# Optimization experiments

Hardware: AMD Instinct MI355X
Metric: run time of the kernel (lower is better)

Reference implementation:

```python
import jax, jax.numpy as jnp
import numpy as np

N, F, H, C, E, DEPTH = 4096, 1433, 32, 7, 131072, 3
RATIO = 0.5

def dense_adj(edge_index, n):
    # undirected, unweighted, no self loops (Planetoid-style graph)
    A = jnp.zeros((n, n), jnp.float32).at[edge_index[0], edge_index[1]].set(1.0)
    A = jnp.maximum(A, A.T)
    return A * (1.0 - jnp.eye(n, dtype=jnp.float32))

def gcn(x, A, W, b):
    # GCNConv(improved=True): A_hat = A + 2I, symmetric degree normalization
    n = A.shape[0]
    Ah = A + 2.0 * jnp.eye(n, dtype=A.dtype)
    deg = Ah.sum(axis=1)
    dinv = jnp.where(deg > 0, jax.lax.rsqrt(deg), 0.0)
    return (dinv[:, None] * Ah * dinv[None, :]) @ (x @ W) + b

def augment(A):
    # PyG GraphUNet.augment_adj: add self loops, A @ A, remove self loops
    n = A.shape[0]
    Ai = A + jnp.eye(n, dtype=A.dtype)
    return (Ai @ Ai) * (1.0 - jnp.eye(n, dtype=A.dtype))

def topk_pool(x, A, p):
    # TopKPooling(ratio=0.5) with tanh score nonlinearity
    score = jnp.tanh((x @ p) / jnp.linalg.norm(p))
    k = int(np.ceil(RATIO * x.shape[0]))  # static under jit
    vals, perm = jax.lax.top_k(score, k)
    return x[perm] * vals[:, None], A[perm][:, perm], perm

def net_forward(x, A, Wi, bi, down_W, down_b, pool_p, up_W, up_b, Wf, bf):
    # eval mode: dropout_adj(p=0.2) and F.dropout(p=0.92) are identity
    x = jax.nn.relu(gcn(x, A, Wi, bi))
    # GraphUNet down path
    h = jax.nn.relu(gcn(x, A, down_W[0], down_b[0]))
    xs, As, perms = [h], [A], []
    cur_A = A
    for i in range(1, DEPTH + 1):
        Aaug = augment(cur_A)
        h, cur_A, perm = topk_pool(h, Aaug, pool_p[i - 1])
        h = jax.nn.relu(gcn(h, cur_A, down_W[i], down_b[i]))
        if i < DEPTH:
            xs.append(h)
            As.append(cur_A)
        perms.append(perm)
    # up path with sum residuals
    for i in range(DEPTH):
        j = DEPTH - 1 - i
        up = jnp.zeros_like(xs[j]).at[perms[j]].set(h)
        h = xs[j] + up
        h = gcn(h, As[j], up_W[i], up_b[i])
        if i < DEPTH - 1:
            h = jax.nn.relu(h)
    x = jax.nn.relu(h)
    out = gcn(x, A, Wf, bf)
    return jax.nn.log_softmax(out, axis=1)

def setup_inputs():
    key = jax.random.key(0)
    ks = jax.random.split(key, 8)
    return {
        "x": jax.random.normal(ks[0], (N, F), dtype=jnp.float32),
        "edge_index": jax.random.randint(ks[1], (2, E), 0, N),
        "Wi": jax.random.normal(ks[2], (F, H), dtype=jnp.float32) / np.float32(np.sqrt(F)),
        "bi": jnp.zeros((H,), jnp.float32),
        "down_W": jax.random.normal(ks[3], (DEPTH + 1, H, H), dtype=jnp.float32) / np.float32(np.sqrt(H)),
        "down_b": jnp.zeros((DEPTH + 1, H), jnp.float32),
        "pool_p": jax.random.normal(ks[4], (DEPTH, H), dtype=jnp.float32),
        "up_W": jax.random.normal(ks[5], (DEPTH, H, H), dtype=jnp.float32) / np.float32(np.sqrt(H)),
        "up_b": jnp.zeros((DEPTH, H), jnp.float32),
        "Wf": jax.random.normal(ks[6], (H, C), dtype=jnp.float32) / np.float32(np.sqrt(H)),
        "bf": jnp.zeros((C,), jnp.float32),
    }

def reference(x, edge_index, Wi, bi, down_W, down_b, pool_p, up_W, up_b, Wf, bf):
    A = dense_adj(edge_index, N)
    return net_forward(x, A, Wi, bi, down_W, down_b, pool_p, up_W, up_b, Wf, bf)
```

## Files before the change

### kernel.cpp

```cpp
#include <hip/hip_runtime.h>
#include <hip/hip_bf16.h>
#include <cstdint>

#define N_NODES 4096
#define F_IN    1433
#define N_EDGE  131072

typedef short short8v __attribute__((ext_vector_type(8)));
typedef float f32x4 __attribute__((ext_vector_type(4)));

#define GLOBAL_AS __attribute__((address_space(1)))
#define LDS_AS    __attribute__((address_space(3)))

__device__ __forceinline__ void gload_lds16(const void* g, void* l) {
  __builtin_amdgcn_global_load_lds((const GLOBAL_AS void*)g, (LDS_AS void*)l, 16, 0, 0);
}

__device__ __forceinline__ float bf16_to_f32(unsigned short u) {
  union { unsigned u; float f; } c;
  c.u = ((unsigned)u) << 16;
  return c.f;
}

__device__ __forceinline__ unsigned short f32_to_bf16_rne(float f) {
  union { float f; unsigned u; } c; c.f = f;
  unsigned u = c.u;
  return (unsigned short)((u + 0x7FFFu + ((u >> 16) & 1u)) >> 16);
}


__global__ void scatter_edges_k(const int* __restrict__ e0, const int* __restrict__ e1,
                                unsigned short* __restrict__ Ab, int n, int ne) {
  int t = blockIdx.x * 256 + threadIdx.x;
  if (t >= ne) return;
  int u = e0[t], v = e1[t];
  if (u != v) {
    Ab[(size_t)u * n + v] = 0x3F80;
    Ab[(size_t)v * n + u] = 0x3F80;
  }
}

__global__ void deg_dinv_bf16_k(const unsigned short* __restrict__ A,
                                float* __restrict__ dinv, int n) {
  int wid  = (blockIdx.x * blockDim.x + threadIdx.x) >> 6;
  int lane = threadIdx.x & 63;
  if (wid >= n) return;
  const unsigned short* row = A + (size_t)wid * n;
  float s = 0.f;
  for (int j = lane * 8; j < n; j += 512) {
    uint4 v = *(const uint4*)(row + j);
    s += bf16_to_f32((unsigned short)(v.x & 0xffff)) + bf16_to_f32((unsigned short)(v.x >> 16));
    s += bf16_to_f32((unsigned short)(v.y & 0xffff)) + bf16_to_f32((unsigned short)(v.y >> 16));
    s += bf16_to_f32((unsigned short)(v.z & 0xffff)) + bf16_to_f32((unsigned short)(v.z >> 16));
    s += bf16_to_f32((unsigned short)(v.w & 0xffff)) + bf16_to_f32((unsigned short)(v.w >> 16));
  }
#pragma unroll
  for (int off = 32; off > 0; off >>= 1) s += __shfl_down(s, off, 64);
  if (lane == 0) {
    float d = s + 2.0f;
    dinv[wid] = d > 0.f ? 1.0f / sqrtf(d) : 0.f;
  }
}

__global__ void deg_dinv_f32_k(const float* __restrict__ A, float* __restrict__ dinv, int n) {
  int wid  = (blockIdx.x * blockDim.x + threadIdx.x) >> 6;
  int lane = threadIdx.x & 63;
  if (wid >= n) return;
  const float* row = A + (size_t)wid * n;
  float s = 0.f;
  for (int j = lane * 4; j < n; j += 256) {
    float4 v = *(const float4*)(row + j);
    s += (v.x + v.y) + (v.z + v.w);
  }
#pragma unroll
  for (int off = 32; off > 0; off >>= 1) s += __shfl_down(s, off, 64);
  if (lane == 0) {
    float d = s + 2.0f;
    dinv[wid] = d > 0.f ? 1.0f / sqrtf(d) : 0.f;
  }
}


__global__ void gather_rows_bf16_k(const unsigned short* __restrict__ src,
                                   const int* __restrict__ perm,
                                   unsigned short* __restrict__ dst, int K, int cbits) {
  size_t t = (size_t)blockIdx.x * 256 + threadIdx.x;
  int r  = (int)(t >> cbits);
  int c8 = (int)(t & ((1u << cbits) - 1));
  uint4 v = *(const uint4*)(src + (size_t)perm[r] * K + c8 * 8);
  *(uint4*)(dst + t * 8) = v;
}

__global__ void gather_rows_f32_k(const float* __restrict__ src,
                                  const int* __restrict__ perm,
                                  float* __restrict__ dst, int K, int cbits) {
  size_t t = (size_t)blockIdx.x * 256 + threadIdx.x;
  int r  = (int)(t >> cbits);
  int c4 = (int)(t & ((1u << cbits) - 1));
  float4 v = *(const float4*)(src + (size_t)perm[r] * K + c4 * 4);
  *(float4*)(dst + t * 4) = v;
}


__device__ __forceinline__ void block_map(int bid, int nb, int& bx, int& by) {
  if (nb == 16) {
    int xcd = bid & 7, idx = bid >> 3;
    by = (xcd >> 1) * 4 + (idx >> 3);
    bx = (xcd & 1) * 8 + (idx & 7);
  } else if (nb == 8) {
    int xcd = bid & 7, idx = bid >> 3;
    by = (xcd >> 1) * 2 + (idx >> 2);
    bx = (xcd & 1) * 4 + (idx & 3);
  } else {
    bx = bid % nb; by = bid / nb;
  }
}

__global__ __launch_bounds__(512) void gemm_bf16_pool_k(
    const __hip_bfloat16* __restrict__ Ap, const int* __restrict__ perm,
    float* __restrict__ outF, unsigned short* __restrict__ outB, int M, int K) {
  __shared__ short lds[2][2][128 * 32];
  int nb = M >> 7;
  int bx, by; block_map(blockIdx.x, nb, bx, by);
  int row0 = by << 7, col0 = bx << 7;
  int tid = threadIdx.x;
  int wv = tid >> 6, ln = tid & 63;
  int lr = ln & 15, kh = ln >> 4;
  int wr = wv >> 2, wc = wv & 3;

  f32x4 acc[4][2] = {};

  auto stage = [&](int buf, int k0) {
#pragma unroll
    for (int t = 0; t < 2; ++t) {
      int rbase = t ? col0 : row0;
      int row = tid >> 2, colb = (tid & 3) * 16;
      const char* g = (const char*)(Ap + (size_t)(rbase + row) * K + k0) + colb;
      gload_lds16(g, (char*)&lds[buf][t][0] + wv * 1024);
    }
  };

  int nt = K >> 5;
  stage(0, 0);
  int cur = 0;
  for (int kt = 0; kt < nt; ++kt) {
    __syncthreads();
    if (kt + 1 < nt) stage(cur ^ 1, (kt + 1) << 5);
    const short* AbL = &lds[cur][0][0];
    const short* BbL = &lds[cur][1][0];
    short8v af[4], bfr[2];
#pragma unroll
    for (int m = 0; m < 4; ++m)
      af[m] = *(const short8v*)(AbL + (wr * 64 + m * 16 + lr) * 32 + kh * 8);
#pragma unroll
    for (int q = 0; q < 2; ++q)
      bfr[q] = *(const short8v*)(BbL + (wc * 32 + q * 16 + lr) * 32 + kh * 8);
#pragma unroll
    for (int m = 0; m < 4; ++m)
#pragma unroll
      for (int q = 0; q < 2; ++q)
        acc[m][q] = __builtin_amdgcn_mfma_f32_16x16x32_bf16(af[m], bfr[q], acc[m][q], 0, 0, 0);
    cur ^= 1;
  }

#pragma unroll
  for (int q = 0; q < 2; ++q) {
    int col = col0 + wc * 32 + q * 16 + lr;
    int pc  = perm[col];
#pragma unroll
    for (int m = 0; m < 4; ++m) {
      int rb = row0 + wr * 64 + m * 16 + kh * 4;
#pragma unroll
      for (int r = 0; r < 4; ++r) {
        int row = rb + r;
        float v = acc[m][q][r] +
                  2.0f * bf16_to_f32(((const unsigned short*)Ap)[(size_t)row * K + pc]);
        if (row == col) v = 0.f;
        if (outF) outF[(size_t)row * M + col] = v;
        if (outB) {
          union { float f; unsigned u; } c2; c2.f = v;
          outB[(size_t)row * M + col] = (unsigned short)(c2.u >> 16);
        }
      }
    }
  }
}


__global__ __launch_bounds__(256) void gemm_f32_pool_k(
    const float* __restrict__ Ap, const int* __restrict__ perm,
    float* __restrict__ outF, int M, int K) {
  __shared__ float As[32][33];
  __shared__ float Bs[32][33];
  int nb = M >> 5;
  int bx = blockIdx.x % nb, by = blockIdx.x / nb;
  int row0 = by << 5, col0 = bx << 5;
  int tid = threadIdx.x;
  int tr = tid >> 4, tc = tid & 15;
  int lr = tid >> 3, lq = (tid & 7) * 4;
  float acc[2][2] = {};
  for (int k0 = 0; k0 < K; k0 += 32) {
    float4 av = *(const float4*)(Ap + (size_t)(row0 + lr) * K + k0 + lq);
    float4 bv = *(const float4*)(Ap + (size_t)(col0 + lr) * K + k0 + lq);
    __syncthreads();
    As[lq + 0][lr] = av.x; As[lq + 1][lr] = av.y;
    As[lq + 2][lr] = av.z; As[lq + 3][lr] = av.w;
    Bs[lq + 0][lr] = bv.x; Bs[lq + 1][lr] = bv.y;
    Bs[lq + 2][lr] = bv.z; Bs[lq + 3][lr] = bv.w;
    __syncthreads();
#pragma unroll
    for (int k = 0; k < 32; ++k) {
      float2 a = *(const float2*)&As[k][tr * 2];
      float2 b = *(const float2*)&Bs[k][tc * 2];
      acc[0][0] += a.x * b.x; acc[0][1] += a.x * b.y;
      acc[1][0] += a.y * b.x; acc[1][1] += a.y * b.y;
    }
  }
#pragma unroll
  for (int j = 0; j < 2; ++j) {
    int col = col0 + tc * 2 + j;
    int pc = perm[col];
#pragma unroll
    for (int i = 0; i < 2; ++i) {
      int row = row0 + tr * 2 + i;
      float v = acc[i][j] + 2.0f * Ap[(size_t)row * K + pc];
      if (row == col) v = 0.f;
      outF[(size_t)row * M + col] = v;
    }
  }
}

template <int K2>
__global__ void xw_scale_k(const float* __restrict__ X, const float* __restrict__ W,
                           const float* __restrict__ dinv, float* __restrict__ Z,
                           int n, int K1, int relu_in) {
  __shared__ float Xs[8][128];
  int tx = threadIdx.x, ty = threadIdx.y;
  int i0 = blockIdx.x * 8;
  int tid = ty * 32 + tx;
  float acc = 0.f;
  for (int k0 = 0; k0 < K1; k0 += 128) {
    __syncthreads();
#pragma unroll
    for (int l = 0; l < 4; ++l) {
      int idx = tid + l * 256;
      int r = idx >> 7, kk = idx & 127;
      float xv = (k0 + kk < K1) ? X[(size_t)(i0 + r) * K1 + k0 + kk] : 0.f;
      if (relu_in) xv = fmaxf(xv, 0.f);
      Xs[r][kk] = xv;
    }
    __syncthreads();
    if (tx < K2) {
      int lim = min(128, K1 - k0);
      for (int kk = 0; kk < lim; ++kk)
        acc += Xs[ty][kk] * W[(size_t)(k0 + kk) * K2 + tx];
    }
  }
  if (tx < K2) Z[(size_t)(i0 + ty) * K2 + tx] = dinv[i0 + ty] * acc;
}


template <int RELU, int PRESCALED>
__global__ __launch_bounds__(256) void xsplit_k(const float* __restrict__ X,
                                                const float* __restrict__ dinv,
                                                unsigned short* __restrict__ T0,
                                                unsigned short* __restrict__ T1,
                                                unsigned short* __restrict__ T2, int n) {
  __shared__ float Xs[64][33];
  int tid = threadIdx.x;
  int i0 = blockIdx.x * 64;
#pragma unroll
  for (int l = 0; l < 2; ++l) {
    int idx = tid + l * 256;
    int r = idx >> 3, c4 = (idx & 7) * 4;
    float4 v = *(const float4*)(X + (size_t)(i0 + r) * 32 + c4);
    if (RELU) {
      v.x = fmaxf(v.x, 0.f); v.y = fmaxf(v.y, 0.f);
      v.z = fmaxf(v.z, 0.f); v.w = fmaxf(v.w, 0.f);
    }
    float s = PRESCALED ? 1.f : dinv[i0 + r];
    Xs[r][c4 + 0] = s * v.x; Xs[r][c4 + 1] = s * v.y;
    Xs[r][c4 + 2] = s * v.z; Xs[r][c4 + 3] = s * v.w;
  }
  __syncthreads();
  int c = tid >> 3, ib = (tid & 7) * 8;
  unsigned h0[4], h1[4], h2[4];
#pragma unroll
  for (int u = 0; u < 8; u += 2) {
    unsigned short a0, a1, b0, b1, c0, c1;
    {
      float v = Xs[ib + u][c];
      a0 = f32_to_bf16_rne(v); float r0 = v - bf16_to_f32(a0);
      b0 = f32_to_bf16_rne(r0); float r1 = r0 - bf16_to_f32(b0);
      c0 = f32_to_bf16_rne(r1);
    }
    {
      float v = Xs[ib + u + 1][c];
      a1 = f32_to_bf16_rne(v); float r0 = v - bf16_to_f32(a1);
      b1 = f32_to_bf16_rne(r0); float r1 = r0 - bf16_to_f32(b1);
      c1 = f32_to_bf16_rne(r1);
    }
    h0[u >> 1] = (unsigned)a0 | ((unsigned)a1 << 16);
    h1[u >> 1] = (unsigned)b0 | ((unsigned)b1 << 16);
    h2[u >> 1] = (unsigned)c0 | ((unsigned)c1 << 16);
  }
  size_t o = (size_t)c * n + i0 + ib;
  *(uint4*)(T0 + o) = make_uint4(h0[0], h0[1], h0[2], h0[3]);
  *(uint4*)(T1 + o) = make_uint4(h1[0], h1[1], h1[2], h1[3]);
  *(uint4*)(T2 + o) = make_uint4(h2[0], h2[1], h2[2], h2[3]);
}


template <int HAS_W, int HCO, int LOGSM>
__global__ __launch_bounds__(512) void agg_mfma_k(
    const unsigned short* __restrict__ Aadj,
    const unsigned short* __restrict__ T0, const unsigned short* __restrict__ T1,
    const unsigned short* __restrict__ T2,
    const float* __restrict__ X, const float* __restrict__ dinv,
    const float* __restrict__ W, const float* __restrict__ bias,
    float* __restrict__ out, int n, int prescaled, int relu_in, int relu_out) {
  __shared__ float yw[8][32][17];
  __shared__ float Ws[32][32];
  __shared__ float ytot[32][17];
  __shared__ float Os[16][8];
  __shared__ float bs[32];
  int tid = threadIdx.x;
  int wv = tid >> 6, ln = tid & 63;
  int lr = ln & 15, kh = ln >> 4;
  int node0 = blockIdx.x * 16;

  if (HAS_W) {
    if (HCO == 32) {
#pragma unroll
      for (int l = 0; l < 2; ++l) {
        int idx = tid + l * 512;
        Ws[idx >> 5][idx & 31] = W[idx];
      }
    } else {
      if (tid < 32 * HCO) Ws[tid / HCO][tid % HCO] = W[tid];
    }
  }
  if (tid < HCO) bs[tid] = bias[tid];

  int kper = n >> 3;
  int kbeg = wv * kper;
  const unsigned short* Ar = Aadj + (size_t)(node0 + lr) * n + kh * 8;
  const unsigned short* t0 = T0 + (size_t)lr * n + kh * 8;
  const unsigned short* t1 = T1 + (size_t)lr * n + kh * 8;
  const unsigned short* t2 = T2 + (size_t)lr * n + kh * 8;
  const size_t m16 = (size_t)16 * n;

  f32x4 acc0 = {0.f, 0.f, 0.f, 0.f}, acc1 = {0.f, 0.f, 0.f, 0.f};
  for (int k = kbeg; k < kbeg + kper; k += 32) {
    short8v b   = *(const short8v*)(Ar + k);
    short8v a00 = *(const short8v*)(t0 + k);
    short8v a01 = *(const short8v*)(t0 + m16 + k);
    short8v a10 = *(const short8v*)(t1 + k);
    short8v a11 = *(const short8v*)(t1 + m16 + k);
    short8v a20 = *(const short8v*)(t2 + k);
    short8v a21 = *(const short8v*)(t2 + m16 + k);
    acc0 = __builtin_amdgcn_mfma_f32_16x16x32_bf16(a00, b, acc0, 0, 0, 0);
    acc1 = __builtin_amdgcn_mfma_f32_16x16x32_bf16(a01, b, acc1, 0, 0, 0);
    acc0 = __builtin_amdgcn_mfma_f32_16x16x32_bf16(a10, b, acc0, 0, 0, 0);
    acc1 = __builtin_amdgcn_mfma_f32_16x16x32_bf16(a11, b, acc1, 0, 0, 0);
    acc0 = __builtin_amdgcn_mfma_f32_16x16x32_bf16(a20, b, acc0, 0, 0, 0);
    acc1 = __builtin_amdgcn_mfma_f32_16x16x32_bf16(a21, b, acc1, 0, 0, 0);
  }
#pragma unroll
  for (int r = 0; r < 4; ++r) {
    yw[wv][kh * 4 + r][lr]      = acc0[r];
    yw[wv][16 + kh * 4 + r][lr] = acc1[r];
  }
  __syncthreads();

  {
    int c = tid >> 4, i = tid & 15;
    float ysum = 0.f;
#pragma unroll
    for (int w = 0; w < 8; ++w) ysum += yw[w][c][i];
    int node = node0 + i;
    float di = dinv[node];
    float xi = X[(size_t)node * 32 + c];
    if (relu_in) xi = fmaxf(xi, 0.f);
    float si = prescaled ? 1.f : di;
    float yt = di * (ysum + 2.f * si * xi);
    if (!HAS_W) {
      yt += bs[c];
      if (relu_out) yt = fmaxf(yt, 0.f);
      out[(size_t)node * 32 + c] = yt;
    } else {
      ytot[c][i] = yt;
    }
  }
  if (!HAS_W) return;
  __syncthreads();

  if (HCO == 32) {
    int i = tid >> 5, cf = tid & 31;
    float o = bs[cf];
#pragma unroll
    for (int c = 0; c < 32; ++c) o += ytot[c][i] * Ws[c][cf];
    if (relu_out) o = fmaxf(o, 0.f);
    out[(size_t)(node0 + i) * 32 + cf] = o;
  } else {
    int i = tid >> 5, cf = tid & 31;
    if (cf < HCO) {
      float o = bs[cf];
#pragma unroll
      for (int c = 0; c < 32; ++c) o += ytot[c][i] * Ws[c][cf];
      Os[i][cf] = o;
    }
    __syncthreads();
    if (LOGSM) {
      if (tid < 16) {
        int node = node0 + tid;
        float m = Os[tid][0];
#pragma unroll
        for (int c2 = 1; c2 < 7; ++c2) m = fmaxf(m, Os[tid][c2]);
        float ss = 0.f;
#pragma unroll
        for (int c2 = 0; c2 < 7; ++c2) ss += expf(Os[tid][c2] - m);
        float ls = logf(ss);
#pragma unroll
        for (int c2 = 0; c2 < 7; ++c2) out[(size_t)node * 7 + c2] = Os[tid][c2] - m - ls;
      }
    } else {
      if (cf < HCO) out[(size_t)(node0 + i) * 7 + cf] = Os[i][cf];
    }
  }
}


template <int BF16A, int HCO, int HAS_W, int LOGSM>
__global__ __launch_bounds__(256) void gcn_fused_k(
    const void* __restrict__ Av, const float* __restrict__ X,
    const float* __restrict__ dinv, const float* __restrict__ W,
    const float* __restrict__ bias, float* __restrict__ out,
    int n, int prescaled, int relu_in, int relu_out) {
  __shared__ float As[16][68];
  __shared__ float Xs[64][32];
  __shared__ float Ws[32][32];
  __shared__ float Ys[16][33];
  __shared__ float Os[16][8];
  __shared__ float bs[32];
  int tid = threadIdx.x;
  int rt = tid >> 4, cg = tid & 15;
  int row0 = blockIdx.x * 16;

  if (HAS_W) {
    if (HCO == 32) {
#pragma unroll
      for (int l = 0; l < 4; ++l) {
        int idx = tid + l * 256;
        Ws[idx >> 5][idx & 31] = W[idx];
      }
    } else {
      if (tid < 32 * HCO) Ws[tid / HCO][tid % HCO] = W[tid];
    }
  }
  if (tid < HCO) bs[tid] = bias[tid];

  float acc0 = 0.f, acc1 = 0.f;
  for (int j0 = 0; j0 < n; j0 += 64) {
    __syncthreads();
    {
      int r = tid >> 4, q = (tid & 15) * 4;
      if (BF16A) {
        ushort4 a4 = *(const ushort4*)((const unsigned short*)Av + (size_t)(row0 + r) * n + j0 + q);
        As[r][q + 0] = bf16_to_f32(a4.x);
        As[r][q + 1] = bf16_to_f32(a4.y);
        As[r][q + 2] = bf16_to_f32(a4.z);
        As[r][q + 3] = bf16_to_f32(a4.w);
      } else {
        *(float4*)&As[r][q] = *(const float4*)((const float*)Av + (size_t)(row0 + r) * n + j0 + q);
      }
    }
#pragma unroll
    for (int l = 0; l < 2; ++l) {
      int f = tid + l * 256;
      int r = f >> 3, q = (f & 7) * 4;
      float4 v = *(const float4*)(X + (size_t)(j0 + r) * 32 + q);
      if (relu_in) {
        v.x = fmaxf(v.x, 0.f); v.y = fmaxf(v.y, 0.f);
        v.z = fmaxf(v.z, 0.f); v.w = fmaxf(v.w, 0.f);
      }
      float s = prescaled ? 1.f : dinv[j0 + r];
      Xs[r][q + 0] = s * v.x; Xs[r][q + 1] = s * v.y;
      Xs[r][q + 2] = s * v.z; Xs[r][q + 3] = s * v.w;
    }
    __syncthreads();
#pragma unroll
    for (int j = 0; j < 64; ++j) {
      float av = As[rt][j];
      float2 zv = *(const float2*)&Xs[j][cg * 2];
      acc0 += av * zv.x;
      acc1 += av * zv.y;
    }
  }

  int row = row0 + rt;
  float di = dinv[row];
  int c0 = cg * 2;
  float xa = X[(size_t)row * 32 + c0], xb = X[(size_t)row * 32 + c0 + 1];
  if (relu_in) { xa = fmaxf(xa, 0.f); xb = fmaxf(xb, 0.f); }
  float s_i = prescaled ? 1.f : di;
  float y0 = di * (acc0 + 2.f * s_i * xa);
  float y1 = di * (acc1 + 2.f * s_i * xb);

  if (!HAS_W) {
    y0 += bs[c0]; y1 += bs[c0 + 1];
    if (relu_out) { y0 = fmaxf(y0, 0.f); y1 = fmaxf(y1, 0.f); }
    *(float2*)(out + (size_t)row * 32 + c0) = make_float2(y0, y1);
    return;
  }

  Ys[rt][c0] = y0; Ys[rt][c0 + 1] = y1;
  __syncthreads();
  if (HCO == 32) {
    float o0 = bs[c0], o1 = bs[c0 + 1];
#pragma unroll
    for (int c = 0; c < 32; ++c) {
      float yv = Ys[rt][c];
      o0 += yv * Ws[c][c0];
      o1 += yv * Ws[c][c0 + 1];
    }
    if (relu_out) { o0 = fmaxf(o0, 0.f); o1 = fmaxf(o1, 0.f); }
    *(float2*)(out + (size_t)row * 32 + c0) = make_float2(o0, o1);
  } else {
    if (cg < HCO) {
      float o = bs[cg];
#pragma unroll
      for (int c = 0; c < 32; ++c) o += Ys[rt][c] * Ws[c][cg];
      Os[rt][cg] = o;
    }
    __syncthreads();
    if (LOGSM) {
      if (cg == 0) {
        float m = Os[rt][0];
#pragma unroll
        for (int c = 1; c < 7; ++c) m = fmaxf(m, Os[rt][c]);
        float ss = 0.f;
#pragma unroll
        for (int c = 0; c < 7; ++c) ss += expf(Os[rt][c] - m);
        float ls = logf(ss);
#pragma unroll
        for (int c = 0; c < 7; ++c) out[(size_t)row * 7 + c] = Os[rt][c] - m - ls;
      }
    } else {
      if (cg < HCO) out[(size_t)row * 7 + cg] = Os[rt][cg];
    }
  }
}


__global__ void score_k(const float* __restrict__ h, const float* __restrict__ p,
                        float* __restrict__ score, int n) {
  int i = blockIdx.x * 256 + threadIdx.x;
  if (i >= n) return;
  float s = 0.f, pn = 0.f;
#pragma unroll
  for (int c = 0; c < 32; ++c) {
    float pc = p[c];
    s += h[(size_t)i * 32 + c] * pc;
    pn += pc * pc;
  }
  score[i] = tanhf(s / sqrtf(pn));
}

__global__ void topk4_k(const float* __restrict__ score, int* __restrict__ perm,
                        float* __restrict__ vals, int* __restrict__ inv, int n, int k) {
  __shared__ float sc[256];
  int tid = threadIdx.x;
  int e = blockIdx.x * 64 + (tid >> 2);
  int part = tid & 3;
  float si = score[e];
  int rank = 0;
  for (int j0 = 0; j0 < n; j0 += 256) {
    __syncthreads();
    sc[tid] = score[j0 + tid];
    __syncthreads();
    int base = part * 64;
#pragma unroll 16
    for (int jj = 0; jj < 64; ++jj) {
      float sj = sc[base + jj];
      int j = j0 + base + jj;
      rank += (sj > si) || ((sj == si) && (j < e));
    }
  }
  rank += __shfl_xor(rank, 1, 64);
  rank += __shfl_xor(rank, 2, 64);
  if (part == 0) {
    inv[e] = (rank < k) ? rank : -1;
    if (rank < k) { perm[rank] = e; vals[rank] = si; }
  }
}

__global__ void pool_h_k(const float* __restrict__ h, const int* __restrict__ perm,
                         const float* __restrict__ vals, float* __restrict__ out, int k) {
  int idx = blockIdx.x * 256 + threadIdx.x;
  if (idx >= k * 32) return;
  int r = idx >> 5, c = idx & 31;
  out[idx] = h[(size_t)perm[r] * 32 + c] * vals[r];
}

__global__ void unpool_add_k(const float* __restrict__ xs, const int* __restrict__ inv,
                             const float* __restrict__ h, float* __restrict__ out, int n) {
  int t = blockIdx.x * 256 + threadIdx.x;
  if (t >= n * 8) return;
  int i = t >> 3, c4 = (t & 7) * 4;
  float4 v = *(const float4*)(xs + (size_t)i * 32 + c4);
  int r = inv[i];
  if (r >= 0) {
    float4 u = *(const float4*)(h + (size_t)r * 32 + c4);
    v.x += u.x; v.y += u.y; v.z += u.z; v.w += u.w;
  }
  *(float4*)(out + (size_t)i * 32 + c4) = v;
}


extern "C" void kernel_launch(void* const* d_in, const int* in_sizes, int n_in,
                              void* d_out, int out_size, void* d_ws, size_t ws_size,
                              hipStream_t stream) {
  (void)in_sizes; (void)n_in; (void)out_size; (void)ws_size;
  const float* x   = (const float*)d_in[0];
  const int*  eidx = (const int*)d_in[1];
  const float* Wi  = (const float*)d_in[2];
  const float* bi  = (const float*)d_in[3];
  const float* dW  = (const float*)d_in[4];
  const float* db  = (const float*)d_in[5];
  const float* pp  = (const float*)d_in[6];
  const float* uW  = (const float*)d_in[7];
  const float* ub  = (const float*)d_in[8];
  const float* Wf  = (const float*)d_in[9];
  const float* bf  = (const float*)d_in[10];
  float* outp = (float*)d_out;

  char* ws = (char*)d_ws;
  size_t off = 0;
  auto alloc = [&](size_t bytes) -> char* {
    char* p = ws + off;
    off += (bytes + 255) & ~(size_t)255;
    return p;
  };
  const int n0 = 4096, n1 = 2048, n2 = 1024, n3 = 512;
  unsigned short* Abf   = (unsigned short*)alloc((size_t)n0 * n0 * 2);
  unsigned short* As1bf = (unsigned short*)alloc((size_t)n1 * n1 * 2);
  float* As2  = (float*)alloc((size_t)n2 * n2 * 4);
  float* A3   = (float*)alloc((size_t)n3 * n3 * 4);
  unsigned short* Ap  = (unsigned short*)alloc((size_t)n1 * n0 * 2);
  unsigned short* Ap2 = (unsigned short*)alloc((size_t)n2 * n1 * 2);
  float* Ap3 = (float*)alloc((size_t)n3 * n2 * 4);
  unsigned short* T0 = (unsigned short*)alloc((size_t)n0 * 32 * 2);
  unsigned short* T1 = (unsigned short*)alloc((size_t)n0 * 32 * 2);
  unsigned short* T2 = (unsigned short*)alloc((size_t)n0 * 32 * 2);
  float* dinv0 = (float*)alloc(n0 * 4);
  float* dinv1 = (float*)alloc(n1 * 4);
  float* dinv2 = (float*)alloc(n2 * 4);
  float* dinv3 = (float*)alloc(n3 * 4);
  float* Zb    = (float*)alloc((size_t)n0 * 32 * 4);
  float* x0    = (float*)alloc((size_t)n0 * 32 * 4);
  float* xs0   = (float*)alloc((size_t)n0 * 32 * 4);
  float* xs1   = (float*)alloc((size_t)n1 * 32 * 4);
  float* xs2   = (float*)alloc((size_t)n2 * 32 * 4);
  float* hA    = (float*)alloc((size_t)n0 * 32 * 4);
  float* hB    = (float*)alloc((size_t)n0 * 32 * 4);
  float* scb   = (float*)alloc(n0 * 4);
  float* valsb = (float*)alloc(n0 * 4);
  int* perm1 = (int*)alloc(n1 * 4);
  int* perm2 = (int*)alloc(n2 * 4);
  int* perm3 = (int*)alloc(n3 * 4);
  int* inv1  = (int*)alloc(n0 * 4);
  int* inv2  = (int*)alloc(n1 * 4);
  int* inv3  = (int*)alloc(n2 * 4);

  hipMemsetAsync(Abf, 0, (size_t)n0 * n0 * 2, stream);
  scatter_edges_k<<<N_EDGE / 256, 256, 0, stream>>>(eidx, eidx + N_EDGE, Abf, n0, N_EDGE);
  deg_dinv_bf16_k<<<n0 / 4, 256, 0, stream>>>(Abf, dinv0, n0);

  xw_scale_k<32><<<n0 / 8, dim3(32, 8), 0, stream>>>(x, Wi, dinv0, Zb, n0, F_IN, 0);
  xsplit_k<0, 1><<<n0 / 64, 256, 0, stream>>>(Zb, dinv0, T0, T1, T2, n0);
  agg_mfma_k<0, 32, 0><<<n0 / 16, 512, 0, stream>>>(Abf, T0, T1, T2, Zb, dinv0, nullptr, bi, x0, n0, 1, 0, 1);
  xsplit_k<0, 0><<<n0 / 64, 256, 0, stream>>>(x0, dinv0, T0, T1, T2, n0);
  agg_mfma_k<1, 32, 0><<<n0 / 16, 512, 0, stream>>>(Abf, T0, T1, T2, x0, dinv0, dW, db, xs0, n0, 0, 0, 1);

  score_k<<<n0 / 256, 256, 0, stream>>>(xs0, pp, scb, n0);
  topk4_k<<<n0 / 64, 256, 0, stream>>>(scb, perm1, valsb, inv1, n0, n1);
  pool_h_k<<<n1 * 32 / 256, 256, 0, stream>>>(xs0, perm1, valsb, hA, n1);
  gather_rows_bf16_k<<<(int)((size_t)n1 * n0 / 8 / 256), 256, 0, stream>>>(Abf, perm1, Ap, n0, 9);
  gemm_bf16_pool_k<<<(n1 / 128) * (n1 / 128), 512, 0, stream>>>(
      (const __hip_bfloat16*)Ap, perm1, nullptr, As1bf, n1, n0);
  deg_dinv_bf16_k<<<n1 / 4, 256, 0, stream>>>(As1bf, dinv1, n1);
  xsplit_k<0, 0><<<n1 / 64, 256, 0, stream>>>(hA, dinv1, T0, T1, T2, n1);
  agg_mfma_k<1, 32, 0><<<n1 / 16, 512, 0, stream>>>(As1bf, T0, T1, T2, hA, dinv1, dW + 1024, db + 32, xs1, n1, 0, 0, 1);

  score_k<<<n1 / 256, 256, 0, stream>>>(xs1, pp + 32, scb, n1);
  topk4_k<<<n1 / 64, 256, 0, stream>>>(scb, perm2, valsb, inv2, n1, n2);
  pool_h_k<<<n2 * 32 / 256, 256, 0, stream>>>(xs1, perm2, valsb, hA, n2);
  gather_rows_bf16_k<<<(int)((size_t)n2 * n1 / 8 / 256), 256, 0, stream>>>(As1bf, perm2, Ap2, n1, 8);
  gemm_bf16_pool_k<<<(n2 / 128) * (n2 / 128), 512, 0, stream>>>(
      (const __hip_bfloat16*)Ap2, perm2, As2, nullptr, n2, n1);
  deg_dinv_f32_k<<<n2 / 4, 256, 0, stream>>>(As2, dinv2, n2);
  gcn_fused_k<0, 32, 1, 0><<<n2 / 16, 256, 0, stream>>>(As2, hA, dinv2, dW + 2048, db + 64, xs2, n2, 0, 0, 1);

  score_k<<<n2 / 256, 256, 0, stream>>>(xs2, pp + 64, scb, n2);
  topk4_k<<<n2 / 64, 256, 0, stream>>>(scb, perm3, valsb, inv3, n2, n3);
  pool_h_k<<<n3 * 32 / 256, 256, 0, stream>>>(xs2, perm3, valsb, hA, n3);
  gather_rows_f32_k<<<(int)((size_t)n3 * n2 / 4 / 256), 256, 0, stream>>>(As2, perm3, Ap3, n2, 8);
  gemm_f32_pool_k<<<(n3 / 32) * (n3 / 32), 256, 0, stream>>>(Ap3, perm3, A3, n3, n2);
  deg_dinv_f32_k<<<n3 / 4, 256, 0, stream>>>(A3, dinv3, n3);
  gcn_fused_k<0, 32, 1, 0><<<n3 / 16, 256, 0, stream>>>(A3, hA, dinv3, dW + 3072, db + 96, hB, n3, 0, 0, 1);

  unpool_add_k<<<n2 / 32, 256, 0, stream>>>(xs2, inv3, hB, hA, n2);
  gcn_fused_k<0, 32, 1, 0><<<n2 / 16, 256, 0, stream>>>(As2, hA, dinv2, uW, ub, hB, n2, 0, 0, 1);

  unpool_add_k<<<n1 / 32, 256, 0, stream>>>(xs1, inv2, hB, hA, n1);
  xsplit_k<0, 0><<<n1 / 64, 256, 0, stream>>>(hA, dinv1, T0, T1, T2, n1);
  agg_mfma_k<1, 32, 0><<<n1 / 16, 512, 0, stream>>>(As1bf, T0, T1, T2, hA, dinv1, uW + 1024, ub + 32, hB, n1, 0, 0, 1);

  unpool_add_k<<<n0 / 32, 256, 0, stream>>>(xs0, inv1, hB, hA, n0);
  xsplit_k<0, 0><<<n0 / 64, 256, 0, stream>>>(hA, dinv0, T0, T1, T2, n0);
  agg_mfma_k<1, 32, 0><<<n0 / 16, 512, 0, stream>>>(Abf, T0, T1, T2, hA, dinv0, uW + 2048, ub + 64, hB, n0, 0, 0, 0);

  xsplit_k<1, 0><<<n0 / 64, 256, 0, stream>>>(hB, dinv0, T0, T1, T2, n0);
  agg_mfma_k<1, 7, 1><<<n0 / 16, 512, 0, stream>>>(Abf, T0, T1, T2, hB, dinv0, Wf, bf, outp, n0, 0, 1, 0);
}
```

Measured before the change: 634.9 us.

## Fuse bf16 split into producer kernels, swizzle pool GEMM LDS, unroll xw

Removes the standalone xsplit kernels. Producers now write the three-way bf16 split (T0/T1/T2) directly: xw_scale, agg_mfma epilogues, pooling and unpool-add, using double-buffered T arrays so producer and consumer do not alias. It also XOR-swizzles the LDS layout in the bf16 pool GEMM to reduce bank conflicts, and uses four independent accumulators in the xw_scale inner loop. Several launches and their round trips through global memory go away. In exchange, epilogues do scattered column-major 2-byte stores, which may be poorly coalesced.

```diff
diff --git a/kernel.cpp b/kernel.cpp
--- a/kernel.cpp
+++ b/kernel.cpp
@@ -26,6 +26,13 @@
   union { float f; unsigned u; } c; c.f = f;
   unsigned u = c.u;
   return (unsigned short)((u + 0x7FFFu + ((u >> 16) & 1u)) >> 16);
+}
+
+__device__ __forceinline__ void split3(float v, unsigned short& a,
+                                       unsigned short& b, unsigned short& c) {
+  a = f32_to_bf16_rne(v); float r0 = v - bf16_to_f32(a);
+  b = f32_to_bf16_rne(r0); float r1 = r0 - bf16_to_f32(b);
+  c = f32_to_bf16_rne(r1);
 }
 
 
@@ -134,12 +141,14 @@
 #pragma unroll
     for (int t = 0; t < 2; ++t) {
       int rbase = t ? col0 : row0;
-      int row = tid >> 2, colb = (tid & 3) * 16;
-      const char* g = (const char*)(Ap + (size_t)(rbase + row) * K + k0) + colb;
+      int row = tid >> 2;
+      int gslot = (tid & 3) ^ ((row >> 1) & 3);
+      const char* g = (const char*)(Ap + (size_t)(rbase + row) * K + k0) + gslot * 16;
       gload_lds16(g, (char*)&lds[buf][t][0] + wv * 1024);
     }
   };
 
+  int sA = kh ^ ((lr >> 1) & 3);
   int nt = K >> 5;
   stage(0, 0);
   int cur = 0;
@@ -151,10 +160,10 @@
     short8v af[4], bfr[2];
 #pragma unroll
     for (int m = 0; m < 4; ++m)
-      af[m] = *(const short8v*)(AbL + (wr * 64 + m * 16 + lr) * 32 + kh * 8);
+      af[m] = *(const short8v*)(AbL + (wr * 64 + m * 16 + lr) * 32 + sA * 8);
 #pragma unroll
     for (int q = 0; q < 2; ++q)
-      bfr[q] = *(const short8v*)(BbL + (wc * 32 + q * 16 + lr) * 32 + kh * 8);
+      bfr[q] = *(const short8v*)(BbL + (wc * 32 + q * 16 + lr) * 32 + sA * 8);
 #pragma unroll
     for (int m = 0; m < 4; ++m)
 #pragma unroll
@@ -230,15 +239,16 @@
   }
 }
 
-template <int K2>
+template <int K2, int EMIT_T>
 __global__ void xw_scale_k(const float* __restrict__ X, const float* __restrict__ W,
                            const float* __restrict__ dinv, float* __restrict__ Z,
-                           int n, int K1, int relu_in) {
+                           unsigned short* __restrict__ T0, unsigned short* __restrict__ T1,
+                           unsigned short* __restrict__ T2, int n, int K1, int relu_in) {
   __shared__ float Xs[8][128];
   int tx = threadIdx.x, ty = threadIdx.y;
   int i0 = blockIdx.x * 8;
   int tid = ty * 32 + tx;
-  float acc = 0.f;
+  float acc0 = 0.f, acc1 = 0.f, acc2 = 0.f, acc3 = 0.f;
   for (int k0 = 0; k0 < K1; k0 += 128) {
     __syncthreads();
 #pragma unroll
@@ -252,73 +262,40 @@
     __syncthreads();
     if (tx < K2) {
       int lim = min(128, K1 - k0);
-      for (int kk = 0; kk < lim; ++kk)
-        acc += Xs[ty][kk] * W[(size_t)(k0 + kk) * K2 + tx];
-    }
-  }
-  if (tx < K2) Z[(size_t)(i0 + ty) * K2 + tx] = dinv[i0 + ty] * acc;
-}
-
-
-template <int RELU, int PRESCALED>
-__global__ __launch_bounds__(256) void xsplit_k(const float* __restrict__ X,
-                                                const float* __restrict__ dinv,
-                                                unsigned short* __restrict__ T0,
-                                                unsigned short* __restrict__ T1,
-                                                unsigned short* __restrict__ T2, int n) {
-  __shared__ float Xs[64][33];
-  int tid = threadIdx.x;
-  int i0 = blockIdx.x * 64;
-#pragma unroll
-  for (int l = 0; l < 2; ++l) {
-    int idx = tid + l * 256;
-    int r = idx >> 3, c4 = (idx & 7) * 4;
-    float4 v = *(const float4*)(X + (size_t)(i0 + r) * 32 + c4);
-    if (RELU) {
-      v.x = fmaxf(v.x, 0.f); v.y = fmaxf(v.y, 0.f);
-      v.z = fmaxf(v.z, 0.f); v.w = fmaxf(v.w, 0.f);
-    }
-    float s = PRESCALED ? 1.f : dinv[i0 + r];
-    Xs[r][c4 + 0] = s * v.x; Xs[r][c4 + 1] = s * v.y;
-    Xs[r][c4 + 2] = s * v.z; Xs[r][c4 + 3] = s * v.w;
-  }
-  __syncthreads();
-  int c = tid >> 3, ib = (tid & 7) * 8;
-  unsigned h0[4], h1[4], h2[4];
-#pragma unroll
-  for (int u = 0; u < 8; u += 2) {
-    unsigned short a0, a1, b0, b1, c0, c1;
-    {
-      float v = Xs[ib + u][c];
-      a0 = f32_to_bf16_rne(v); float r0 = v - bf16_to_f32(a0);
-      b0 = f32_to_bf16_rne(r0); float r1 = r0 - bf16_to_f32(b0);
-      c0 = f32_to_bf16_rne(r1);
-    }
-    {
-      float v = Xs[ib + u + 1][c];
-      a1 = f32_to_bf16_rne(v); float r0 = v - bf16_to_f32(a1);
-      b1 = f32_to_bf16_rne(r0); float r1 = r0 - bf16_to_f32(b1);
-      c1 = f32_to_bf16_rne(r1);
-    }
-    h0[u >> 1] = (unsigned)a0 | ((unsigned)a1 << 16);
-    h1[u >> 1] = (unsigned)b0 | ((unsigned)b1 << 16);
-    h2[u >> 1] = (unsigned)c0 | ((unsigned)c1 << 16);
-  }
-  size_t o = (size_t)c * n + i0 + ib;
-  *(uint4*)(T0 + o) = make_uint4(h0[0], h0[1], h0[2], h0[3]);
-  *(uint4*)(T1 + o) = make_uint4(h1[0], h1[1], h1[2], h1[3]);
-  *(uint4*)(T2 + o) = make_uint4(h2[0], h2[1], h2[2], h2[3]);
-}
-
-
-template <int HAS_W, int HCO, int LOGSM>
+      int kk = 0;
+      for (; kk + 3 < lim; kk += 4) {
+        acc0 += Xs[ty][kk + 0] * W[(size_t)(k0 + kk + 0) * K2 + tx];
+        acc1 += Xs[ty][kk + 1] * W[(size_t)(k0 + kk + 1) * K2 + tx];
+        acc2 += Xs[ty][kk + 2] * W[(size_t)(k0 + kk + 2) * K2 + tx];
+        acc3 += Xs[ty][kk + 3] * W[(size_t)(k0 + kk + 3) * K2 + tx];
+      }
+      for (; kk < lim; ++kk)
+        acc0 += Xs[ty][kk] * W[(size_t)(k0 + kk) * K2 + tx];
+    }
+  }
+  if (tx < K2) {
+    float z = dinv[i0 + ty] * ((acc0 + acc1) + (acc2 + acc3));
+    Z[(size_t)(i0 + ty) * K2 + tx] = z;
+    if (EMIT_T) {
+      unsigned short a, b, c; split3(z, a, b, c);
+      size_t o = (size_t)tx * n + i0 + ty;
+      T0[o] = a; T1[o] = b; T2[o] = c;
+    }
+  }
+}
+
+
+template <int HAS_W, int HCO, int LOGSM, int EMIT_T, int EMIT_RELU>
 __global__ __launch_bounds__(512) void agg_mfma_k(
     const unsigned short* __restrict__ Aadj,
     const unsigned short* __restrict__ T0, const unsigned short* __restrict__ T1,
     const unsigned short* __restrict__ T2,
     const float* __restrict__ X, const float* __restrict__ dinv,
     const float* __restrict__ W, const float* __restrict__ bias,
-    float* __restrict__ out, int n, int prescaled, int relu_in, int relu_out) {
+    float* __restrict__ out,
+    unsigned short* __restrict__ To0, unsigned short* __restrict__ To1,
+    unsigned short* __restrict__ To2,
+    int n, int prescaled, int relu_in, int relu_out) {
   __shared__ float yw[8][32][17];
   __shared__ float Ws[32][32];
   __shared__ float ytot[32][17];
@@ -388,6 +365,11 @@
       yt += bs[c];
       if (relu_out) yt = fmaxf(yt, 0.f);
       out[(size_t)node * 32 + c] = yt;
+      if (EMIT_T) {
+        unsigned short a, b2, c2; split3(di * yt, a, b2, c2);
+        size_t o = (size_t)c * n + node;
+        To0[o] = a; To1[o] = b2; To2[o] = c2;
+      }
     } else {
       ytot[c][i] = yt;
     }
@@ -400,8 +382,15 @@
     float o = bs[cf];
 #pragma unroll
     for (int c = 0; c < 32; ++c) o += ytot[c][i] * Ws[c][cf];
-    if (relu_out) o = fmaxf(o, 0.f);
-    out[(size_t)(node0 + i) * 32 + cf] = o;
+    float ow = relu_out ? fmaxf(o, 0.f) : o;
+    out[(size_t)(node0 + i) * 32 + cf] = ow;
+    if (EMIT_T) {
+      float oT = (EMIT_RELU || relu_out) ? fmaxf(o, 0.f) : o;
+      float di = dinv[node0 + i];
+      unsigned short a, b2, c2; split3(di * oT, a, b2, c2);
+      size_t oidx = (size_t)cf * n + node0 + i;
+      To0[oidx] = a; To1[oidx] = b2; To2[oidx] = c2;
+    }
   } else {
     int i = tid >> 5, cf = tid & 31;
     if (cf < HCO) {
@@ -603,6 +592,21 @@
   out[idx] = h[(size_t)perm[r] * 32 + c] * vals[r];
 }
 
+__global__ void pool_h_split_k(const float* __restrict__ h, const int* __restrict__ perm,
+                               const float* __restrict__ vals, const float* __restrict__ dinv,
+                               float* __restrict__ out,
+                               unsigned short* __restrict__ T0, unsigned short* __restrict__ T1,
+                               unsigned short* __restrict__ T2, int k) {
+  int idx = blockIdx.x * 256 + threadIdx.x;
+  if (idx >= k * 32) return;
+  int r = idx >> 5, c = idx & 31;
+  float v = h[(size_t)perm[r] * 32 + c] * vals[r];
+  out[idx] = v;
+  unsigned short a, b, cc; split3(dinv[r] * v, a, b, cc);
+  size_t o = (size_t)c * k + r;
+  T0[o] = a; T1[o] = b; T2[o] = cc;
+}
+
 __global__ void unpool_add_k(const float* __restrict__ xs, const int* __restrict__ inv,
                              const float* __restrict__ h, float* __restrict__ out, int n) {
   int t = blockIdx.x * 256 + threadIdx.x;
@@ -615,6 +619,31 @@
     v.x += u.x; v.y += u.y; v.z += u.z; v.w += u.w;
   }
   *(float4*)(out + (size_t)i * 32 + c4) = v;
+}
+
+__global__ void unpool_add_split_k(const float* __restrict__ xs, const int* __restrict__ inv,
+                                   const float* __restrict__ h, const float* __restrict__ dinv,
+                                   float* __restrict__ out,
+                                   unsigned short* __restrict__ T0, unsigned short* __restrict__ T1,
+                                   unsigned short* __restrict__ T2, int n) {
+  int t = blockIdx.x * 256 + threadIdx.x;
+  if (t >= n * 8) return;
+  int i = t >> 3, c4 = (t & 7) * 4;
+  float4 v = *(const float4*)(xs + (size_t)i * 32 + c4);
+  int r = inv[i];
+  if (r >= 0) {
+    float4 u = *(const float4*)(h + (size_t)r * 32 + c4);
+    v.x += u.x; v.y += u.y; v.z += u.z; v.w += u.w;
+  }
+  *(float4*)(out + (size_t)i * 32 + c4) = v;
+  float di = dinv[i];
+  float vv[4] = {v.x, v.y, v.z, v.w};
+#pragma unroll
+  for (int j = 0; j < 4; ++j) {
+    unsigned short a, b, cc; split3(di * vv[j], a, b, cc);
+    size_t o = (size_t)(c4 + j) * n + i;
+    T0[o] = a; T1[o] = b; T2[o] = cc;
+  }
 }
 
 
@@ -650,9 +679,12 @@
   unsigned short* Ap  = (unsigned short*)alloc((size_t)n1 * n0 * 2);
   unsigned short* Ap2 = (unsigned short*)alloc((size_t)n2 * n1 * 2);
   float* Ap3 = (float*)alloc((size_t)n3 * n2 * 4);
-  unsigned short* T0 = (unsigned short*)alloc((size_t)n0 * 32 * 2);
-  unsigned short* T1 = (unsigned short*)alloc((size_t)n0 * 32 * 2);
-  unsigned short* T2 = (unsigned short*)alloc((size_t)n0 * 32 * 2);
+  unsigned short* TA0 = (unsigned short*)alloc((size_t)n0 * 32 * 2);
+  unsigned short* TA1 = (unsigned short*)alloc((size_t)n0 * 32 * 2);
+  unsigned short* TA2 = (unsigned short*)alloc((size_t)n0 * 32 * 2);
+  unsigned short* TB0 = (unsigned short*)alloc((size_t)n0 * 32 * 2);
+  unsigned short* TB1 = (unsigned short*)alloc((size_t)n0 * 32 * 2);
+  unsigned short* TB2 = (unsigned short*)alloc((size_t)n0 * 32 * 2);
   float* dinv0 = (float*)alloc(n0 * 4);
   float* dinv1 = (float*)alloc(n1 * 4);
   float* dinv2 = (float*)alloc(n2 * 4);
@@ -677,21 +709,21 @@
   scatter_edges_k<<<N_EDGE / 256, 256, 0, stream>>>(eidx, eidx + N_EDGE, Abf, n0, N_EDGE);
   deg_dinv_bf16_k<<<n0 / 4, 256, 0, stream>>>(Abf, dinv0, n0);
 
-  xw_scale_k<32><<<n0 / 8, dim3(32, 8), 0, stream>>>(x, Wi, dinv0, Zb, n0, F_IN, 0);
-  xsplit_k<0, 1><<<n0 / 64, 256, 0, stream>>>(Zb, dinv0, T0, T1, T2, n0);
-  agg_mfma_k<0, 32, 0><<<n0 / 16, 512, 0, stream>>>(Abf, T0, T1, T2, Zb, dinv0, nullptr, bi, x0, n0, 1, 0, 1);
-  xsplit_k<0, 0><<<n0 / 64, 256, 0, stream>>>(x0, dinv0, T0, T1, T2, n0);
-  agg_mfma_k<1, 32, 0><<<n0 / 16, 512, 0, stream>>>(Abf, T0, T1, T2, x0, dinv0, dW, db, xs0, n0, 0, 0, 1);
+  xw_scale_k<32, 1><<<n0 / 8, dim3(32, 8), 0, stream>>>(x, Wi, dinv0, Zb, TA0, TA1, TA2, n0, F_IN, 0);
+  agg_mfma_k<0, 32, 0, 1, 0><<<n0 / 16, 512, 0, stream>>>(
+      Abf, TA0, TA1, TA2, Zb, dinv0, nullptr, bi, x0, TB0, TB1, TB2, n0, 1, 0, 1);
+  agg_mfma_k<1, 32, 0, 0, 0><<<n0 / 16, 512, 0, stream>>>(
+      Abf, TB0, TB1, TB2, x0, dinv0, dW, db, xs0, nullptr, nullptr, nullptr, n0, 0, 0, 1);
 
   score_k<<<n0 / 256, 256, 0, stream>>>(xs0, pp, scb, n0);
   topk4_k<<<n0 / 64, 256, 0, stream>>>(scb, perm1, valsb, inv1, n0, n1);
-  pool_h_k<<<n1 * 32 / 256, 256, 0, stream>>>(xs0, perm1, valsb, hA, n1);
   gather_rows_bf16_k<<<(int)((size_t)n1 * n0 / 8 / 256), 256, 0, stream>>>(Abf, perm1, Ap, n0, 9);
   gemm_bf16_pool_k<<<(n1 / 128) * (n1 / 128), 512, 0, stream>>>(
       (const __hip_bfloat16*)Ap, perm1, nullptr, As1bf, n1, n0);
   deg_dinv_bf16_k<<<n1 / 4, 256, 0, stream>>>(As1bf, dinv1, n1);
-  xsplit_k<0, 0><<<n1 / 64, 256, 0, stream>>>(hA, dinv1, T0, T1, T2, n1);
-  agg_mfma_k<1, 32, 0><<<n1 / 16, 512, 0, stream>>>(As1bf, T0, T1, T2, hA, dinv1, dW + 1024, db + 32, xs1, n1, 0, 0, 1);
+  pool_h_split_k<<<n1 * 32 / 256, 256, 0, stream>>>(xs0, perm1, valsb, dinv1, hA, TA0, TA1, TA2, n1);
+  agg_mfma_k<1, 32, 0, 0, 0><<<n1 / 16, 512, 0, stream>>>(
+      As1bf, TA0, TA1, TA2, hA, dinv1, dW + 1024, db + 32, xs1, nullptr, nullptr, nullptr, n1, 0, 0, 1);
 
   score_k<<<n1 / 256, 256, 0, stream>>>(xs1, pp + 32, scb, n1);
   topk4_k<<<n1 / 64, 256, 0, stream>>>(scb, perm2, valsb, inv2, n1, n2);
@@ -713,14 +745,14 @@
   unpool_add_k<<<n2 / 32, 256, 0, stream>>>(xs2, inv3, hB, hA, n2);
   gcn_fused_k<0, 32, 1, 0><<<n2 / 16, 256, 0, stream>>>(As2, hA, dinv2, uW, ub, hB, n2, 0, 0, 1);
 
-  unpool_add_k<<<n1 / 32, 256, 0, stream>>>(xs1, inv2, hB, hA, n1);
-  xsplit_k<0, 0><<<n1 / 64, 256, 0, stream>>>(hA, dinv1, T0, T1, T2, n1);
-  agg_mfma_k<1, 32, 0><<<n1 / 16, 512, 0, stream>>>(As1bf, T0, T1, T2, hA, dinv1, uW + 1024, ub + 32, hB, n1, 0, 0, 1);
-
-  unpool_add_k<<<n0 / 32, 256, 0, stream>>>(xs0, inv1, hB, hA, n0);
-  xsplit_k<0, 0><<<n0 / 64, 256, 0, stream>>>(hA, dinv0, T0, T1, T2, n0);
-  agg_mfma_k<1, 32, 0><<<n0 / 16, 512, 0, stream>>>(Abf, T0, T1, T2, hA, dinv0, uW + 2048, ub + 64, hB, n0, 0, 0, 0);
-
-  xsplit_k<1, 0><<<n0 / 64, 256, 0, stream>>>(hB, dinv0, T0, T1, T2, n0);
-  agg_mfma_k<1, 7, 1><<<n0 / 16, 512, 0, stream>>>(Abf, T0, T1, T2, hB, dinv0, Wf, bf, outp, n0, 0, 1, 0);
-}
+  unpool_add_split_k<<<n1 / 32, 256, 0, stream>>>(xs1, inv2, hB, dinv1, hA, TA0, TA1, TA2, n1);
+  agg_mfma_k<1, 32, 0, 0, 0><<<n1 / 16, 512, 0, stream>>>(
+      As1bf, TA0, TA1, TA2, hA, dinv1, uW + 1024, ub + 32, hB, nullptr, nullptr, nullptr, n1, 0, 0, 1);
+
+  unpool_add_split_k<<<n0 / 32, 256, 0, stream>>>(xs0, inv1, hB, dinv0, hA, TA0, TA1, TA2, n0);
+  agg_mfma_k<1, 32, 0, 1, 1><<<n0 / 16, 512, 0, stream>>>(
+      Abf, TA0, TA1, TA2, hA, dinv0, uW + 2048, ub + 64, hB, TB0, TB1, TB2, n0, 0, 0, 0);
+
+  agg_mfma_k<1, 7, 1, 0, 0><<<n0 / 16, 512, 0, stream>>>(
+      Abf, TB0, TB1, TB2, hB, dinv0, Wf, bf, outp, nullptr, nullptr, nullptr, n0, 0, 1, 0);
+}
```

Result: slower. 654.3 us (+3.1%).
